# Performance work log

Hardware: AMD Instinct MI355X
Metric: run time of the kernel (lower is better)

Reference implementation:

```python
import jax, jax.numpy as jnp
import numpy as np

EPS = 1e-5
N_CONV = 3
B = 2048  # number of crystals


def _bn_eval(x, gamma, beta):
    # Eval-mode BatchNorm with running_mean=0, running_var=1.
    return x * (gamma / jnp.sqrt(1.0 + EPS)) + beta


def _conv_layer(atom_fea, nbr_fea, nbr_fea_idx, W, b, g1, b1, g2, b2):
    # Canonical CGCNN ConvLayer.
    N, M = nbr_fea_idx.shape
    F = atom_fea.shape[1]
    nbr_atom = atom_fea[nbr_fea_idx]                                  # [N,M,F]
    self_atom = jnp.broadcast_to(atom_fea[:, None, :], (N, M, F))     # [N,M,F]
    total = jnp.concatenate([self_atom, nbr_atom, nbr_fea], axis=2)   # [N,M,2F+nbr]
    gated = total @ W + b                                             # [N,M,2F]
    gated = _bn_eval(gated, g1, b1)
    flt, core = jnp.split(gated, 2, axis=2)
    nbr_sumed = jnp.sum(jax.nn.sigmoid(flt) * jax.nn.softplus(core), axis=1)  # [N,F]
    nbr_sumed = _bn_eval(nbr_sumed, g2, b2)
    return jax.nn.softplus(atom_fea + nbr_sumed)


def setup_inputs() -> dict:
    key = jax.random.key(0)
    ks = jax.random.split(key, 24)
    N, M = 60000, 12
    OA, NB, F, OE, E, H = 92, 41, 64, 8, 16, 128
    s = 0.05
    inp = {
        "atom_fea": jax.random.normal(ks[0], (N, OA), jnp.float32),
        "nbr_fea": jax.random.normal(ks[1], (N, M, NB), jnp.float32),
        "nbr_fea_idx": jax.random.randint(ks[2], (N, M), 0, N),
        "segment_ids": jnp.sort(jax.random.randint(ks[3], (N,), 0, B)),
        "extra_fea": jax.random.normal(ks[4], (B, OE), jnp.float32),
        # embedding_atom
        "W_embed": jax.random.normal(ks[5], (OA, F), jnp.float32) * s,
        "b_embed": jnp.zeros((F,), jnp.float32),
        # conv layers (stacked over n_conv=3)
        "conv_W": jax.random.normal(ks[6], (N_CONV, 2 * F + NB, 2 * F), jnp.float32) * s,
        "conv_b": jnp.zeros((N_CONV, 2 * F), jnp.float32),
        "bn1_g": jnp.ones((N_CONV, 2 * F), jnp.float32),
        "bn1_b": jnp.zeros((N_CONV, 2 * F), jnp.float32),
        "bn2_g": jnp.ones((N_CONV, F), jnp.float32),
        "bn2_b": jnp.zeros((N_CONV, F), jnp.float32),
        # embedding_extra
        "W_extra": jax.random.normal(ks[7], (OE, E), jnp.float32) * s,
        "b_extra": jnp.zeros((E,), jnp.float32),
        "bnx_g": jnp.ones((E,), jnp.float32),
        "bnx_b": jnp.zeros((E,), jnp.float32),
        # conv_to_fc
        "W_fc": jax.random.normal(ks[8], (F + E, H), jnp.float32) * s,
        "b_fc": jnp.zeros((H,), jnp.float32),
        "W_out0": jax.random.normal(ks[9], (H, 1), jnp.float32) * s,
        "b_out0": jnp.zeros((1,), jnp.float32),
        "W_out1": jax.random.normal(ks[10], (H, 2), jnp.float32) * s,
        "b_out1": jnp.zeros((2,), jnp.float32),
        "W_out2": jax.random.normal(ks[11], (H, 1), jnp.float32) * s,
        "b_out2": jnp.zeros((1,), jnp.float32),
    }
    return inp


def reference(atom_fea, nbr_fea, nbr_fea_idx, segment_ids, extra_fea,
              W_embed, b_embed, conv_W, conv_b, bn1_g, bn1_b, bn2_g, bn2_b,
              W_extra, b_extra, bnx_g, bnx_b, W_fc, b_fc,
              W_out0, b_out0, W_out1, b_out1, W_out2, b_out2):
    x = atom_fea @ W_embed + b_embed                                  # [N,F]
    extra = jax.nn.softplus(_bn_eval(extra_fea @ W_extra + b_extra, bnx_g, bnx_b))  # [B,E]
    for i in range(N_CONV):
        x = _conv_layer(x, nbr_fea, nbr_fea_idx, conv_W[i], conv_b[i],
                        bn1_g[i], bn1_b[i], bn2_g[i], bn2_b[i])
    # segment-mean pooling (replaces per-crystal python loop)
    sums = jax.ops.segment_sum(x, segment_ids, num_segments=B)        # [B,F]
    cnts = jax.ops.segment_sum(jnp.ones((x.shape[0],), x.dtype), segment_ids, num_segments=B)
    crys = sums / jnp.maximum(cnts, 1.0)[:, None]
    crys = jnp.concatenate([crys, extra], axis=1)                     # [B,F+E]
    crys = jax.nn.softplus(crys @ W_fc + b_fc)                        # [B,H]
    out0 = crys @ W_out0 + b_out0
    out1 = jax.nn.log_softmax(crys @ W_out1 + b_out1, axis=1)         # classification [B,2]
    out2 = crys @ W_out2 + b_out2
    return out0, out1, out2
```

## Files before the change

kernel.cpp:

```cpp
#include <hip/hip_runtime.h>
#include <math.h>
#include <stdint.h>

#define N_ATOMS 60000
#define M_NBR   12
#define NBF     41
#define B_CRYS  2048
#define EPSBN   1e-5f
#define GA      8
#define ROWS    (GA * M_NBR)
#define GRID_F  (N_ATOMS / GA)
#define WIMG_L  24576
#define EROW    48
#define EP_ROWS (GRID_F * ROWS)

#define PRE_WP   288
#define PRE_EMB  960
#define PRE_EPR  2048

typedef __attribute__((ext_vector_type(8))) short bf8;
typedef __attribute__((ext_vector_type(4))) float f32x4;
#define MFMA_B16(a, b, c) __builtin_amdgcn_mfma_f32_16x16x32_bf16(a, b, c, 0, 0, 0)

__device__ __forceinline__ short f2bf(float f) {
  uint32_t u = __builtin_bit_cast(uint32_t, f);
  u += 0x7FFFu + ((u >> 16) & 1u);
  return (short)(u >> 16);
}
__device__ __forceinline__ float lo16(uint32_t u) {
  return __builtin_bit_cast(float, u << 16);
}
__device__ __forceinline__ float hi16(uint32_t u) {
  return __builtin_bit_cast(float, u & 0xFFFF0000u);
}
__device__ __forceinline__ float sp(float x) {
  return (x > 15.f) ? x : __logf(1.f + __expf(x));
}
__device__ __forceinline__ float sig(float x) {
  return 1.f / (1.f + __expf(-x));
}

__global__ __launch_bounds__(256) void k_pre(
    const float* __restrict__ conv_W, const float* __restrict__ conv_b,
    const float* __restrict__ bn1_g, const float* __restrict__ bn1_b,
    unsigned short* __restrict__ Wimg, const float* __restrict__ A,
    const float* __restrict__ W, const float* __restrict__ bias,
    float* __restrict__ X, unsigned int* __restrict__ XbU,
    const float* __restrict__ NF, unsigned short* __restrict__ Eimg,
    int do_eprep) {
  const int b = blockIdx.x;

  if (b < PRE_WP) {
    const int gid = b * 256 + threadIdx.x;
    if (gid >= 3 * WIMG_L) return;
    const int layer = gid / WIMG_L, rem = gid % WIMG_L;
    const int which = rem / 8192, r2 = rem % 8192;
    const int frag = r2 >> 9, lane = (r2 >> 3) & 63, j = r2 & 7;
    const int ct = frag >> 1, ks = frag & 1;
    const int quad = lane >> 4, l15 = lane & 15;
    const int jc = ct * 16 + l15;
    const int oc = (jc & 1) ? (jc >> 1) + 64 : (jc >> 1);
    const float s = bn1_g[layer * 128 + oc] * rsqrtf(1.f + EPSBN);
    const int k = ks * 32 + quad * 8 + j;
    const float* Wc = conv_W + (size_t)layer * 169 * 128;
    float v = 0.f;
    if (which == 0) {
      if (k < NBF) v = Wc[(128 + k) * 128 + oc] * s;
      else if (k == NBF)
        v = conv_b[layer * 128 + oc] * s + bn1_b[layer * 128 + oc];
    } else if (which == 1) {
      v = Wc[k * 128 + oc] * s;
    } else {
      v = Wc[(64 + k) * 128 + oc] * s;
    }
    Wimg[gid] = (unsigned short)f2bf(v);
    return;
  }

  if (b < PRE_WP + PRE_EMB) {
    const int lane = threadIdx.x & 63, wv = threadIdx.x >> 6;
    const int quad = lane >> 4, l15 = lane & 15;
    const int gw = (b - PRE_WP) * 4 + wv;
    const int nw = PRE_EMB * 4;
    bf8 Bf[3][4];
    float bs[4];
#pragma unroll
    for (int ct = 0; ct < 4; ++ct) {
      const int col = ct * 16 + l15;
      bs[ct] = bias[col];
#pragma unroll
      for (int ks = 0; ks < 3; ++ks) {
        bf8 bb;
#pragma unroll
        for (int i = 0; i < 8; ++i) {
          const int k = ks * 32 + quad * 8 + i;
          bb[i] = (k < 92) ? f2bf(W[k * 64 + col]) : (short)0;
        }
        Bf[ks][ct] = bb;
      }
    }
    for (int rt = gw; rt < 3750; rt += nw) {
      const int rbase = rt * 16;
      const float* ar = A + (size_t)(rbase + l15) * 92;
      const float4 p0 = *(const float4*)(ar + quad * 8);
      const float4 p1 = *(const float4*)(ar + quad * 8 + 4);
      const float4 p2 = *(const float4*)(ar + 32 + quad * 8);
      const float4 p3 = *(const float4*)(ar + 32 + quad * 8 + 4);
      bf8 A0, A1, A2;
      A0[0] = f2bf(p0.x); A0[1] = f2bf(p0.y); A0[2] = f2bf(p0.z); A0[3] = f2bf(p0.w);
      A0[4] = f2bf(p1.x); A0[5] = f2bf(p1.y); A0[6] = f2bf(p1.z); A0[7] = f2bf(p1.w);
      A1[0] = f2bf(p2.x); A1[1] = f2bf(p2.y); A1[2] = f2bf(p2.z); A1[3] = f2bf(p2.w);
      A1[4] = f2bf(p3.x); A1[5] = f2bf(p3.y); A1[6] = f2bf(p3.z); A1[7] = f2bf(p3.w);
#pragma unroll
      for (int i = 0; i < 8; ++i) {
        const int k = 64 + quad * 8 + i;
        A2[i] = (k < 92) ? f2bf(ar[k]) : (short)0;
      }
      const f32x4 z = {0.f, 0.f, 0.f, 0.f};
      f32x4 acc[4];
#pragma unroll
      for (int ct = 0; ct < 4; ++ct) {
        acc[ct] = MFMA_B16(A0, Bf[0][ct], z);
        acc[ct] = MFMA_B16(A1, Bf[1][ct], acc[ct]);
        acc[ct] = MFMA_B16(A2, Bf[2][ct], acc[ct]);
      }
#pragma unroll
      for (int ct = 0; ct < 4; ++ct)
#pragma unroll
        for (int r = 0; r < 4; ++r) {
          const int row = rbase + quad * 4 + r;
          const float v = acc[ct][r] + bs[ct];
          X[(size_t)row * 64 + ct * 16 + l15] = v;
          const unsigned int u = (unsigned short)f2bf(v);
          const unsigned int p = __shfl_xor((int)u, 1);
          if (!(l15 & 1))
            XbU[(size_t)row * 32 + ct * 8 + (l15 >> 1)] = u | (p << 16);
        }
    }
    return;
  }

  if (!do_eprep) return;
  const int t0 = (b - PRE_WP - PRE_EMB) * 256 + threadIdx.x;
  for (int r = t0; r < EP_ROWS; r += PRE_EPR * 256) {
    const float* rp = NF + (size_t)r * NBF;
    unsigned short* op = Eimg + (size_t)r * EROW;
#pragma unroll
    for (int g8 = 0; g8 < 5; ++g8) {
      bf8 v;
#pragma unroll
      for (int i = 0; i < 8; ++i) v[i] = f2bf(rp[g8 * 8 + i]);
      *(bf8*)(op + g8 * 8) = v;
    }
    bf8 v5;
    v5[0] = f2bf(rp[40]);
    v5[1] = (short)0x3F80;
#pragma unroll
    for (int i = 2; i < 8; ++i) v5[i] = 0;
    *(bf8*)(op + 40) = v5;
  }
}

__global__ __launch_bounds__(256, 5) void k_fused6(
    float* __restrict__ X, const unsigned short* __restrict__ XbIn,
    unsigned int* __restrict__ XbOutU, const unsigned short* __restrict__ Eimg,
    const int* __restrict__ IDX, const unsigned short* __restrict__ Wi,
    const float* __restrict__ g2, const float* __restrict__ b2) {
  __shared__ __align__(16) unsigned int eb32[ROWS * 64];
  unsigned short* eb16 = (unsigned short*)eb32;
  const int tid = threadIdx.x;
  const int lane = tid & 63, wv = tid >> 6;
  const int quad = lane >> 4, l15 = lane & 15;
  const int g = blockIdx.x;
  const int ntile = (wv < 2) ? 2 : 1;

  bf8 Ax0[2], Ax1[2], As0[2], As1[2], Ae0[2], Ae1[2];
#pragma unroll
  for (int ti = 0; ti < 2; ++ti) {
    if (ti < ntile) {
      const int rbase = (wv + ti * 4) * 16;
      const int er = g * ROWS + rbase + l15;
      const int jr = IDX[er];
      const unsigned short* xr = XbIn + (size_t)jr * 64 + quad * 8;
      Ax0[ti] = *(const bf8*)xr;
      Ax1[ti] = *(const bf8*)(xr + 32);
      const int arow = g * GA + (rbase + l15) / M_NBR;
      const unsigned short* sr = XbIn + (size_t)arow * 64 + quad * 8;
      As0[ti] = *(const bf8*)sr;
      As1[ti] = *(const bf8*)(sr + 32);
      const unsigned short* ep = Eimg + (size_t)er * EROW;
      Ae0[ti] = *(const bf8*)(ep + quad * 8);
      bf8 a1;
#pragma unroll
      for (int i = 0; i < 8; ++i) a1[i] = 0;
      if (quad < 2) a1 = *(const bf8*)(ep + 32 + quad * 8);
      Ae1[ti] = a1;
    }
  }

#pragma unroll
  for (int ti = 0; ti < 2; ++ti) {
    if (ti < ntile) {
      const int rbase = (wv + ti * 4) * 16;
      const f32x4 z = {0.f, 0.f, 0.f, 0.f};
#pragma unroll 1
      for (int ct = 0; ct < 8; ++ct) {
        const bf8 Be0 = *(const bf8*)(Wi + ((ct * 2 + 0) * 64 + lane) * 8);
        const bf8 Be1 = *(const bf8*)(Wi + ((ct * 2 + 1) * 64 + lane) * 8);
        const bf8 Bs0 =
            *(const bf8*)(Wi + 8192 + ((ct * 2 + 0) * 64 + lane) * 8);
        const bf8 Bs1 =
            *(const bf8*)(Wi + 8192 + ((ct * 2 + 1) * 64 + lane) * 8);
        const bf8 Bn0 =
            *(const bf8*)(Wi + 16384 + ((ct * 2 + 0) * 64 + lane) * 8);
        const bf8 Bn1 =
            *(const bf8*)(Wi + 16384 + ((ct * 2 + 1) * 64 + lane) * 8);
        f32x4 acc = MFMA_B16(Ax0[ti], Bn0, z);
        acc = MFMA_B16(Ax1[ti], Bn1, acc);
        acc = MFMA_B16(As0[ti], Bs0, acc);
        acc = MFMA_B16(As1[ti], Bs1, acc);
        acc = MFMA_B16(Ae0[ti], Be0, acc);
        acc = MFMA_B16(Ae1[ti], Be1, acc);
        const int j = ct * 16 + l15;
        const int c = j >> 1, h = j & 1;
#pragma unroll
        for (int r = 0; r < 4; ++r) {
          const int row = rbase + quad * 4 + r;
          eb16[row * 128 + ((c + row) & 63) * 2 + h] =
              (unsigned short)f2bf(acc[r]);
        }
      }
    }
  }
  __syncthreads();

  const float inv = rsqrtf(1.f + EPSBN);
  const float s2 = g2[lane] * inv, o2 = b2[lane];
#pragma unroll
  for (int al = 0; al < 2; ++al) {
    const int a_local = wv * 2 + al;
    const int n = g * GA + a_local;
    float acc = 0.f;
#pragma unroll
    for (int m = 0; m < 12; ++m) {
      const int row = a_local * 12 + m;
      const uint32_t eu = eb32[row * 64 + ((lane + row) & 63)];
      acc += sig(lo16(eu)) * sp(hi16(eu));
    }
    const size_t o = (size_t)n * 64 + lane;
    const float res = sp(X[o] + acc * s2 + o2);
    X[o] = res;
    const unsigned int u = (unsigned short)f2bf(res);
    const unsigned int p = __shfl_xor((int)u, 1);
    if (!(lane & 1)) XbOutU[(size_t)n * 32 + (lane >> 1)] = u | (p << 16);
  }
}

__global__ __launch_bounds__(256, 5) void k_fused4(
    float* __restrict__ X, const unsigned short* __restrict__ XbIn,
    unsigned int* __restrict__ XbOutU, const float* __restrict__ NF,
    const int* __restrict__ IDX, const unsigned short* __restrict__ Wi,
    const float* __restrict__ g2, const float* __restrict__ b2) {
  __shared__ __align__(16) unsigned int eb32[ROWS * 64];
  unsigned short* eb16 = (unsigned short*)eb32;
  float* stage = (float*)eb32;
  const int tid = threadIdx.x;
  const int lane = tid & 63, wv = tid >> 6;
  const int quad = lane >> 4, l15 = lane & 15;
  const int g = blockIdx.x;
  const int ntile = (wv < 2) ? 2 : 1;

  bf8 Ax0[2], Ax1[2], As0[2], As1[2];
#pragma unroll
  for (int ti = 0; ti < 2; ++ti) {
    if (ti < ntile) {
      const int rbase = (wv + ti * 4) * 16;
      const int jr = IDX[g * ROWS + rbase + l15];
      const unsigned short* xr = XbIn + (size_t)jr * 64 + quad * 8;
      Ax0[ti] = *(const bf8*)xr;
      Ax1[ti] = *(const bf8*)(xr + 32);
      const int arow = g * GA + (rbase + l15) / M_NBR;
      const unsigned short* sr = XbIn + (size_t)arow * 64 + quad * 8;
      As0[ti] = *(const bf8*)sr;
      As1[ti] = *(const bf8*)(sr + 32);
    }
  }

  const float4* s4 = (const float4*)(NF + (size_t)g * (ROWS * NBF));
#pragma unroll
  for (int it = 0; it < 4; ++it) {
    const int w = tid + it * 256;
    if (w < (ROWS * NBF) / 4) ((float4*)stage)[w] = s4[w];
  }
  __syncthreads();

  bf8 Ae0[2], Ae1[2];
#pragma unroll
  for (int ti = 0; ti < 2; ++ti) {
    if (ti < ntile) {
      const int rbase = (wv + ti * 4) * 16;
      const float* rp = stage + (rbase + l15) * NBF;
      bf8 a0, a1;
#pragma unroll
      for (int i = 0; i < 8; ++i) a0[i] = f2bf(rp[quad * 8 + i]);
      if (quad == 0) {
#pragma unroll
        for (int i = 0; i < 8; ++i) a1[i] = f2bf(rp[32 + i]);
      } else if (quad == 1) {
        a1[0] = f2bf(rp[40]);
        a1[1] = (short)0x3F80;
#pragma unroll
        for (int i = 2; i < 8; ++i) a1[i] = 0;
      } else {
#pragma unroll
        for (int i = 0; i < 8; ++i) a1[i] = 0;
      }
      Ae0[ti] = a0;
      Ae1[ti] = a1;
    }
  }
  __syncthreads();

#pragma unroll
  for (int ti = 0; ti < 2; ++ti) {
    if (ti < ntile) {
      const int rbase = (wv + ti * 4) * 16;
      const f32x4 z = {0.f, 0.f, 0.f, 0.f};
#pragma unroll 1
      for (int ct = 0; ct < 8; ++ct) {
        const bf8 Be0 = *(const bf8*)(Wi + ((ct * 2 + 0) * 64 + lane) * 8);
        const bf8 Be1 = *(const bf8*)(Wi + ((ct * 2 + 1) * 64 + lane) * 8);
        const bf8 Bs0 =
            *(const bf8*)(Wi + 8192 + ((ct * 2 + 0) * 64 + lane) * 8);
        const bf8 Bs1 =
            *(const bf8*)(Wi + 8192 + ((ct * 2 + 1) * 64 + lane) * 8);
        const bf8 Bn0 =
            *(const bf8*)(Wi + 16384 + ((ct * 2 + 0) * 64 + lane) * 8);
        const bf8 Bn1 =
            *(const bf8*)(Wi + 16384 + ((ct * 2 + 1) * 64 + lane) * 8);
        f32x4 acc = MFMA_B16(Ax0[ti], Bn0, z);
        acc = MFMA_B16(Ax1[ti], Bn1, acc);
        acc = MFMA_B16(As0[ti], Bs0, acc);
        acc = MFMA_B16(As1[ti], Bs1, acc);
        acc = MFMA_B16(Ae0[ti], Be0, acc);
        acc = MFMA_B16(Ae1[ti], Be1, acc);
        const int j = ct * 16 + l15;
        const int c = j >> 1, h = j & 1;
#pragma unroll
        for (int r = 0; r < 4; ++r) {
          const int row = rbase + quad * 4 + r;
          eb16[row * 128 + ((c + row) & 63) * 2 + h] =
              (unsigned short)f2bf(acc[r]);
        }
      }
    }
  }
  __syncthreads();

  const float inv = rsqrtf(1.f + EPSBN);
  const float s2 = g2[lane] * inv, o2 = b2[lane];
#pragma unroll
  for (int al = 0; al < 2; ++al) {
    const int a_local = wv * 2 + al;
    const int n = g * GA + a_local;
    float acc = 0.f;
#pragma unroll
    for (int m = 0; m < 12; ++m) {
      const int row = a_local * 12 + m;
      const uint32_t eu = eb32[row * 64 + ((lane + row) & 63)];
      acc += sig(lo16(eu)) * sp(hi16(eu));
    }
    const size_t o = (size_t)n * 64 + lane;
    const float res = sp(X[o] + acc * s2 + o2);
    X[o] = res;
    const unsigned int u = (unsigned short)f2bf(res);
    const unsigned int p = __shfl_xor((int)u, 1);
    if (!(lane & 1)) XbOutU[(size_t)n * 32 + (lane >> 1)] = u | (p << 16);
  }
}

__device__ __forceinline__ int lbound(const int* __restrict__ a, int n, int v) {
  int lo = 0, hi = n;
  while (lo < hi) {
    int mid = (lo + hi) >> 1;
    if (a[mid] < v) lo = mid + 1; else hi = mid;
  }
  return lo;
}

__global__ __launch_bounds__(128) void k_head(
    const float* __restrict__ Xf, const int* __restrict__ seg,
    const float* __restrict__ EF, const float* __restrict__ Wx,
    const float* __restrict__ bx, const float* __restrict__ gx,
    const float* __restrict__ bxb, const float* __restrict__ Wfc,
    const float* __restrict__ bfc, const float* __restrict__ Wo0,
    const float* __restrict__ bo0, const float* __restrict__ Wo1,
    const float* __restrict__ bo1, const float* __restrict__ Wo2,
    const float* __restrict__ bo2, float* __restrict__ out) {
  const int b = blockIdx.x;
  const int t = threadIdx.x;
  __shared__ float vbuf[80];
  __shared__ float part[128];
  __shared__ float4 r4[128];
  const int lo = lbound(seg, N_ATOMS, b);
  const int hi = lbound(seg, N_ATOMS, b + 1);
  const int col = t & 63, half = t >> 6;
  float s = 0.f;
  for (int r = lo + half; r < hi; r += 2) s += Xf[(size_t)r * 64 + col];
  part[t] = s;
  __syncthreads();
  if (t < 64) {
    vbuf[t] = (part[t] + part[t + 64]) / fmaxf((float)(hi - lo), 1.f);
  } else if (t < 80) {
    const int e = t - 64;
    float a = bx[e];
#pragma unroll
    for (int k = 0; k < 8; ++k) a += EF[b * 8 + k] * Wx[k * 16 + e];
    a = a * (gx[e] * rsqrtf(1.f + EPSBN)) + bxb[e];
    vbuf[t] = sp(a);
  }
  __syncthreads();
  float h = bfc[t];
#pragma unroll
  for (int k = 0; k < 80; ++k) h += vbuf[k] * Wfc[k * 128 + t];
  h = sp(h);
  r4[t] = make_float4(h * Wo0[t], h * Wo1[2 * t], h * Wo1[2 * t + 1],
                      h * Wo2[t]);
  __syncthreads();
  for (int st2 = 64; st2 > 0; st2 >>= 1) {
    if (t < st2) {
      float4 a = r4[t], c = r4[t + st2];
      r4[t] = make_float4(a.x + c.x, a.y + c.y, a.z + c.z, a.w + c.w);
    }
    __syncthreads();
  }
  if (t == 0) {
    float4 r = r4[0];
    out[b] = r.x + bo0[0];
    float z0 = r.y + bo1[0], z1 = r.z + bo1[1];
    float mx = fmaxf(z0, z1);
    float lse = mx + __logf(__expf(z0 - mx) + __expf(z1 - mx));
    out[B_CRYS + 2 * b] = z0 - lse;
    out[B_CRYS + 2 * b + 1] = z1 - lse;
    out[3 * B_CRYS + b] = r.w + bo2[0];
  }
}

extern "C" void kernel_launch(void* const* d_in, const int* in_sizes, int n_in,
                              void* d_out, int out_size, void* d_ws,
                              size_t ws_size, hipStream_t stream) {
  const float* atom_fea = (const float*)d_in[0];
  const float* nbr_fea  = (const float*)d_in[1];
  const int*   nbr_idx  = (const int*)d_in[2];
  const int*   seg      = (const int*)d_in[3];
  const float* extra    = (const float*)d_in[4];
  const float* W_embed  = (const float*)d_in[5];
  const float* b_embed  = (const float*)d_in[6];
  const float* conv_W   = (const float*)d_in[7];
  const float* conv_b   = (const float*)d_in[8];
  const float* bn1_g    = (const float*)d_in[9];
  const float* bn1_b    = (const float*)d_in[10];
  const float* bn2_g    = (const float*)d_in[11];
  const float* bn2_b    = (const float*)d_in[12];
  const float* W_extra  = (const float*)d_in[13];
  const float* b_extra  = (const float*)d_in[14];
  const float* bnx_g    = (const float*)d_in[15];
  const float* bnx_b    = (const float*)d_in[16];
  const float* W_fc     = (const float*)d_in[17];
  const float* b_fc     = (const float*)d_in[18];
  const float* W_out0   = (const float*)d_in[19];
  const float* b_out0   = (const float*)d_in[20];
  const float* W_out1   = (const float*)d_in[21];
  const float* b_out1   = (const float*)d_in[22];
  const float* W_out2   = (const float*)d_in[23];
  const float* b_out2   = (const float*)d_in[24];
  float* out = (float*)d_out;

  float* x = (float*)d_ws;
  unsigned int* xbu0 = (unsigned int*)(x + (size_t)N_ATOMS * 64);
  unsigned int* xbu1 = xbu0 + (size_t)N_ATOMS * 32;
  unsigned short* Wimg = (unsigned short*)(xbu1 + (size_t)N_ATOMS * 32);
  unsigned short* Eimg = Wimg + (size_t)3 * WIMG_L;

  const size_t base_bytes =
      (size_t)N_ATOMS * 64 * 4 + (size_t)N_ATOMS * 32 * 4 * 2 +
      (size_t)3 * WIMG_L * 2;
  const size_t eimg_bytes = (size_t)EP_ROWS * EROW * 2;
  const bool use_eimg = (ws_size >= base_bytes + eimg_bytes);

  const int pre_grid =
      use_eimg ? (PRE_WP + PRE_EMB + PRE_EPR) : (PRE_WP + PRE_EMB);
  hipLaunchKernelGGL(k_pre, dim3(pre_grid), dim3(256), 0, stream, conv_W,
                     conv_b, bn1_g, bn1_b, Wimg, atom_fea, W_embed, b_embed, x,
                     xbu0, nbr_fea, Eimg, (int)use_eimg);

  unsigned int* xin = xbu0;
  unsigned int* xout = xbu1;
  for (int i = 0; i < 3; ++i) {
    if (use_eimg) {
      hipLaunchKernelGGL(k_fused6, dim3(GRID_F), dim3(256), 0, stream, x,
                         (const unsigned short*)xin, xout, Eimg, nbr_idx,
                         Wimg + (size_t)i * WIMG_L, bn2_g + i * 64,
                         bn2_b + i * 64);
    } else {
      hipLaunchKernelGGL(k_fused4, dim3(GRID_F), dim3(256), 0, stream, x,
                         (const unsigned short*)xin, xout, nbr_fea, nbr_idx,
                         Wimg + (size_t)i * WIMG_L, bn2_g + i * 64,
                         bn2_b + i * 64);
    }
    unsigned int* tmp = xin;
    xin = xout;
    xout = tmp;
  }
  hipLaunchKernelGGL(k_head, dim3(B_CRYS), dim3(128), 0, stream, x, seg, extra,
                     W_extra, b_extra, bnx_g, bnx_b, W_fc, b_fc, W_out0, b_out0,
                     W_out1, b_out1, W_out2, b_out2, out);
}
```

Measured before the change: 556.6 us.

## Fuse segment-mean pooling into last conv layer via atomics

```diff
diff --git a/kernel.cpp b/kernel.cpp
--- a/kernel.cpp
+++ b/kernel.cpp
@@ -14,9 +14,11 @@
 #define EROW    48
 #define EP_ROWS (GRID_F * ROWS)
 
+#define PRE_EPR  2048
 #define PRE_WP   288
 #define PRE_EMB  960
-#define PRE_EPR  2048
+#define PRE_Z    64
+#define PRE_GRID (PRE_EPR + PRE_WP + PRE_EMB + PRE_Z)
 
 typedef __attribute__((ext_vector_type(8))) short bf8;
 typedef __attribute__((ext_vector_type(4))) float f32x4;
@@ -47,11 +49,34 @@
     const float* __restrict__ W, const float* __restrict__ bias,
     float* __restrict__ X, unsigned int* __restrict__ XbU,
     const float* __restrict__ NF, unsigned short* __restrict__ Eimg,
-    int do_eprep) {
+    float* __restrict__ Xsum, int do_eprep) {
   const int b = blockIdx.x;
 
-  if (b < PRE_WP) {
-    const int gid = b * 256 + threadIdx.x;
+  if (b < PRE_EPR) {
+    if (!do_eprep) return;
+    const int t0 = b * 256 + threadIdx.x;
+    for (int r = t0; r < EP_ROWS; r += PRE_EPR * 256) {
+      const float* rp = NF + (size_t)r * NBF;
+      unsigned short* op = Eimg + (size_t)r * EROW;
+#pragma unroll
+      for (int g8 = 0; g8 < 5; ++g8) {
+        bf8 v;
+#pragma unroll
+        for (int i = 0; i < 8; ++i) v[i] = f2bf(rp[g8 * 8 + i]);
+        *(bf8*)(op + g8 * 8) = v;
+      }
+      bf8 v5;
+      v5[0] = f2bf(rp[40]);
+      v5[1] = (short)0x3F80;
+#pragma unroll
+      for (int i = 2; i < 8; ++i) v5[i] = 0;
+      *(bf8*)(op + 40) = v5;
+    }
+    return;
+  }
+
+  if (b < PRE_EPR + PRE_WP) {
+    const int gid = (b - PRE_EPR) * 256 + threadIdx.x;
     if (gid >= 3 * WIMG_L) return;
     const int layer = gid / WIMG_L, rem = gid % WIMG_L;
     const int which = rem / 8192, r2 = rem % 8192;
@@ -77,10 +102,10 @@
     return;
   }
 
-  if (b < PRE_WP + PRE_EMB) {
+  if (b < PRE_EPR + PRE_WP + PRE_EMB) {
     const int lane = threadIdx.x & 63, wv = threadIdx.x >> 6;
     const int quad = lane >> 4, l15 = lane & 15;
-    const int gw = (b - PRE_WP) * 4 + wv;
+    const int gw = (b - PRE_EPR - PRE_WP) * 4 + wv;
     const int nw = PRE_EMB * 4;
     bf8 Bf[3][4];
     float bs[4];
@@ -141,31 +166,18 @@
   }
 
   if (!do_eprep) return;
-  const int t0 = (b - PRE_WP - PRE_EMB) * 256 + threadIdx.x;
-  for (int r = t0; r < EP_ROWS; r += PRE_EPR * 256) {
-    const float* rp = NF + (size_t)r * NBF;
-    unsigned short* op = Eimg + (size_t)r * EROW;
-#pragma unroll
-    for (int g8 = 0; g8 < 5; ++g8) {
-      bf8 v;
-#pragma unroll
-      for (int i = 0; i < 8; ++i) v[i] = f2bf(rp[g8 * 8 + i]);
-      *(bf8*)(op + g8 * 8) = v;
-    }
-    bf8 v5;
-    v5[0] = f2bf(rp[40]);
-    v5[1] = (short)0x3F80;
-#pragma unroll
-    for (int i = 2; i < 8; ++i) v5[i] = 0;
-    *(bf8*)(op + 40) = v5;
-  }
-}
-
-__global__ __launch_bounds__(256, 5) void k_fused6(
+  const int zi = (b - PRE_EPR - PRE_WP - PRE_EMB) * 256 + threadIdx.x;
+  for (int i = zi; i < B_CRYS * 64 + B_CRYS; i += PRE_Z * 256) Xsum[i] = 0.f;
+}
+
+template <int FIN>
+__global__ __launch_bounds__(256, 5) void k_fused6t(
     float* __restrict__ X, const unsigned short* __restrict__ XbIn,
     unsigned int* __restrict__ XbOutU, const unsigned short* __restrict__ Eimg,
     const int* __restrict__ IDX, const unsigned short* __restrict__ Wi,
-    const float* __restrict__ g2, const float* __restrict__ b2) {
+    const float* __restrict__ g2, const float* __restrict__ b2,
+    const int* __restrict__ SEG, float* __restrict__ Xsum,
+    float* __restrict__ CntF) {
   __shared__ __align__(16) unsigned int eb32[ROWS * 64];
   unsigned short* eb16 = (unsigned short*)eb32;
   const int tid = threadIdx.x;
@@ -249,10 +261,16 @@
     }
     const size_t o = (size_t)n * 64 + lane;
     const float res = sp(X[o] + acc * s2 + o2);
-    X[o] = res;
-    const unsigned int u = (unsigned short)f2bf(res);
-    const unsigned int p = __shfl_xor((int)u, 1);
-    if (!(lane & 1)) XbOutU[(size_t)n * 32 + (lane >> 1)] = u | (p << 16);
+    if (FIN) {
+      const int s = SEG[n];
+      atomicAdd(&Xsum[(size_t)s * 64 + lane], res);
+      if (lane == 0) atomicAdd(&CntF[s], 1.f);
+    } else {
+      X[o] = res;
+      const unsigned int u = (unsigned short)f2bf(res);
+      const unsigned int p = __shfl_xor((int)u, 1);
+      if (!(lane & 1)) XbOutU[(size_t)n * 32 + (lane >> 1)] = u | (p << 16);
+    }
   }
 }
 
@@ -396,28 +414,42 @@
     const float* __restrict__ bfc, const float* __restrict__ Wo0,
     const float* __restrict__ bo0, const float* __restrict__ Wo1,
     const float* __restrict__ bo1, const float* __restrict__ Wo2,
-    const float* __restrict__ bo2, float* __restrict__ out) {
+    const float* __restrict__ bo2, const float* __restrict__ Xsum,
+    const float* __restrict__ CntF, int pooled, float* __restrict__ out) {
   const int b = blockIdx.x;
   const int t = threadIdx.x;
   __shared__ float vbuf[80];
   __shared__ float part[128];
   __shared__ float4 r4[128];
-  const int lo = lbound(seg, N_ATOMS, b);
-  const int hi = lbound(seg, N_ATOMS, b + 1);
-  const int col = t & 63, half = t >> 6;
-  float s = 0.f;
-  for (int r = lo + half; r < hi; r += 2) s += Xf[(size_t)r * 64 + col];
-  part[t] = s;
-  __syncthreads();
-  if (t < 64) {
-    vbuf[t] = (part[t] + part[t + 64]) / fmaxf((float)(hi - lo), 1.f);
-  } else if (t < 80) {
-    const int e = t - 64;
-    float a = bx[e];
-#pragma unroll
-    for (int k = 0; k < 8; ++k) a += EF[b * 8 + k] * Wx[k * 16 + e];
-    a = a * (gx[e] * rsqrtf(1.f + EPSBN)) + bxb[e];
-    vbuf[t] = sp(a);
+  if (pooled) {
+    if (t < 64) {
+      vbuf[t] = Xsum[(size_t)b * 64 + t] / fmaxf(CntF[b], 1.f);
+    } else if (t < 80) {
+      const int e = t - 64;
+      float a = bx[e];
+#pragma unroll
+      for (int k = 0; k < 8; ++k) a += EF[b * 8 + k] * Wx[k * 16 + e];
+      a = a * (gx[e] * rsqrtf(1.f + EPSBN)) + bxb[e];
+      vbuf[t] = sp(a);
+    }
+  } else {
+    const int lo = lbound(seg, N_ATOMS, b);
+    const int hi = lbound(seg, N_ATOMS, b + 1);
+    const int col = t & 63, half = t >> 6;
+    float s = 0.f;
+    for (int r = lo + half; r < hi; r += 2) s += Xf[(size_t)r * 64 + col];
+    part[t] = s;
+    __syncthreads();
+    if (t < 64) {
+      vbuf[t] = (part[t] + part[t + 64]) / fmaxf((float)(hi - lo), 1.f);
+    } else if (t < 80) {
+      const int e = t - 64;
+      float a = bx[e];
+#pragma unroll
+      for (int k = 0; k < 8; ++k) a += EF[b * 8 + k] * Wx[k * 16 + e];
+      a = a * (gx[e] * rsqrtf(1.f + EPSBN)) + bxb[e];
+      vbuf[t] = sp(a);
+    }
   }
   __syncthreads();
   float h = bfc[t];
@@ -480,28 +512,35 @@
   unsigned int* xbu0 = (unsigned int*)(x + (size_t)N_ATOMS * 64);
   unsigned int* xbu1 = xbu0 + (size_t)N_ATOMS * 32;
   unsigned short* Wimg = (unsigned short*)(xbu1 + (size_t)N_ATOMS * 32);
-  unsigned short* Eimg = Wimg + (size_t)3 * WIMG_L;
+  float* xsum = (float*)(Wimg + (size_t)3 * WIMG_L);
+  float* cntf = xsum + (size_t)B_CRYS * 64;
+  unsigned short* Eimg = (unsigned short*)(cntf + B_CRYS);
 
   const size_t base_bytes =
       (size_t)N_ATOMS * 64 * 4 + (size_t)N_ATOMS * 32 * 4 * 2 +
-      (size_t)3 * WIMG_L * 2;
+      (size_t)3 * WIMG_L * 2 + (size_t)(B_CRYS * 64 + B_CRYS) * 4;
   const size_t eimg_bytes = (size_t)EP_ROWS * EROW * 2;
   const bool use_eimg = (ws_size >= base_bytes + eimg_bytes);
 
-  const int pre_grid =
-      use_eimg ? (PRE_WP + PRE_EMB + PRE_EPR) : (PRE_WP + PRE_EMB);
-  hipLaunchKernelGGL(k_pre, dim3(pre_grid), dim3(256), 0, stream, conv_W,
+  hipLaunchKernelGGL(k_pre, dim3(PRE_GRID), dim3(256), 0, stream, conv_W,
                      conv_b, bn1_g, bn1_b, Wimg, atom_fea, W_embed, b_embed, x,
-                     xbu0, nbr_fea, Eimg, (int)use_eimg);
+                     xbu0, nbr_fea, Eimg, xsum, (int)use_eimg);
 
   unsigned int* xin = xbu0;
   unsigned int* xout = xbu1;
   for (int i = 0; i < 3; ++i) {
     if (use_eimg) {
-      hipLaunchKernelGGL(k_fused6, dim3(GRID_F), dim3(256), 0, stream, x,
-                         (const unsigned short*)xin, xout, Eimg, nbr_idx,
-                         Wimg + (size_t)i * WIMG_L, bn2_g + i * 64,
-                         bn2_b + i * 64);
+      if (i < 2) {
+        hipLaunchKernelGGL(k_fused6t<0>, dim3(GRID_F), dim3(256), 0, stream, x,
+                           (const unsigned short*)xin, xout, Eimg, nbr_idx,
+                           Wimg + (size_t)i * WIMG_L, bn2_g + i * 64,
+                           bn2_b + i * 64, seg, xsum, cntf);
+      } else {
+        hipLaunchKernelGGL(k_fused6t<1>, dim3(GRID_F), dim3(256), 0, stream, x,
+                           (const unsigned short*)xin, xout, Eimg, nbr_idx,
+                           Wimg + (size_t)i * WIMG_L, bn2_g + i * 64,
+                           bn2_b + i * 64, seg, xsum, cntf);
+      }
     } else {
       hipLaunchKernelGGL(k_fused4, dim3(GRID_F), dim3(256), 0, stream, x,
                          (const unsigned short*)xin, xout, nbr_fea, nbr_idx,
@@ -514,5 +553,6 @@
   }
   hipLaunchKernelGGL(k_head, dim3(B_CRYS), dim3(128), 0, stream, x, seg, extra,
                      W_extra, b_extra, bnx_g, bnx_b, W_fc, b_fc, W_out0, b_out0,
-                     W_out1, b_out1, W_out2, b_out2, out);
-}
+                     W_out1, b_out1, W_out2, b_out2, xsum, cntf, (int)use_eimg,
+                     out);
+}
```

Result: slower. 571.7 us (+2.7%).

## Split bf16 edge prep into finer chunks, precompute segment bounds, widen head

Applied to the files above, without the earlier changes.

```diff
diff --git a/kernel.cpp b/kernel.cpp
--- a/kernel.cpp
+++ b/kernel.cpp
@@ -13,10 +13,13 @@
 #define WIMG_L  24576
 #define EROW    48
 #define EP_ROWS (GRID_F * ROWS)
-
+#define EP_CHUNKS (EP_ROWS * 6)
+
+#define PRE_EPR  2048
 #define PRE_WP   288
 #define PRE_EMB  960
-#define PRE_EPR  2048
+#define PRE_B    9
+#define PRE_GRID (PRE_EPR + PRE_WP + PRE_EMB + PRE_B)
 
 typedef __attribute__((ext_vector_type(8))) short bf8;
 typedef __attribute__((ext_vector_type(4))) float f32x4;
@@ -38,6 +41,14 @@
 }
 __device__ __forceinline__ float sig(float x) {
   return 1.f / (1.f + __expf(-x));
+}
+__device__ __forceinline__ int lbound(const int* __restrict__ a, int n, int v) {
+  int lo = 0, hi = n;
+  while (lo < hi) {
+    int mid = (lo + hi) >> 1;
+    if (a[mid] < v) lo = mid + 1; else hi = mid;
+  }
+  return lo;
 }
 
 __global__ __launch_bounds__(256) void k_pre(
@@ -47,11 +58,33 @@
     const float* __restrict__ W, const float* __restrict__ bias,
     float* __restrict__ X, unsigned int* __restrict__ XbU,
     const float* __restrict__ NF, unsigned short* __restrict__ Eimg,
-    int do_eprep) {
+    const int* __restrict__ seg, int* __restrict__ bounds, int do_eprep) {
   const int b = blockIdx.x;
 
-  if (b < PRE_WP) {
-    const int gid = b * 256 + threadIdx.x;
+  if (b < PRE_EPR) {
+    if (!do_eprep) return;
+    const int t0 = b * 256 + threadIdx.x;
+    for (int c = t0; c < EP_CHUNKS; c += PRE_EPR * 256) {
+      const int row = c / 6, sg = c - row * 6;
+      const float* rp = NF + (size_t)row * NBF + sg * 8;
+      unsigned short* op = Eimg + (size_t)row * EROW + sg * 8;
+      bf8 v;
+      if (sg < 5) {
+#pragma unroll
+        for (int i = 0; i < 8; ++i) v[i] = f2bf(rp[i]);
+      } else {
+        v[0] = f2bf(rp[0]);
+        v[1] = (short)0x3F80;
+#pragma unroll
+        for (int i = 2; i < 8; ++i) v[i] = 0;
+      }
+      *(bf8*)op = v;
+    }
+    return;
+  }
+
+  if (b < PRE_EPR + PRE_WP) {
+    const int gid = (b - PRE_EPR) * 256 + threadIdx.x;
     if (gid >= 3 * WIMG_L) return;
     const int layer = gid / WIMG_L, rem = gid % WIMG_L;
     const int which = rem / 8192, r2 = rem % 8192;
@@ -77,10 +110,10 @@
     return;
   }
 
-  if (b < PRE_WP + PRE_EMB) {
+  if (b < PRE_EPR + PRE_WP + PRE_EMB) {
     const int lane = threadIdx.x & 63, wv = threadIdx.x >> 6;
     const int quad = lane >> 4, l15 = lane & 15;
-    const int gw = (b - PRE_WP) * 4 + wv;
+    const int gw = (b - PRE_EPR - PRE_WP) * 4 + wv;
     const int nw = PRE_EMB * 4;
     bf8 Bf[3][4];
     float bs[4];
@@ -140,25 +173,8 @@
     return;
   }
 
-  if (!do_eprep) return;
-  const int t0 = (b - PRE_WP - PRE_EMB) * 256 + threadIdx.x;
-  for (int r = t0; r < EP_ROWS; r += PRE_EPR * 256) {
-    const float* rp = NF + (size_t)r * NBF;
-    unsigned short* op = Eimg + (size_t)r * EROW;
-#pragma unroll
-    for (int g8 = 0; g8 < 5; ++g8) {
-      bf8 v;
-#pragma unroll
-      for (int i = 0; i < 8; ++i) v[i] = f2bf(rp[g8 * 8 + i]);
-      *(bf8*)(op + g8 * 8) = v;
-    }
-    bf8 v5;
-    v5[0] = f2bf(rp[40]);
-    v5[1] = (short)0x3F80;
-#pragma unroll
-    for (int i = 2; i < 8; ++i) v5[i] = 0;
-    *(bf8*)(op + 40) = v5;
-  }
+  const int bi = (b - PRE_EPR - PRE_WP - PRE_EMB) * 256 + threadIdx.x;
+  if (bi <= B_CRYS) bounds[bi] = lbound(seg, N_ATOMS, bi);
 }
 
 __global__ __launch_bounds__(256, 5) void k_fused6(
@@ -379,17 +395,8 @@
   }
 }
 
-__device__ __forceinline__ int lbound(const int* __restrict__ a, int n, int v) {
-  int lo = 0, hi = n;
-  while (lo < hi) {
-    int mid = (lo + hi) >> 1;
-    if (a[mid] < v) lo = mid + 1; else hi = mid;
-  }
-  return lo;
-}
-
-__global__ __launch_bounds__(128) void k_head(
-    const float* __restrict__ Xf, const int* __restrict__ seg,
+__global__ __launch_bounds__(256) void k_head(
+    const float* __restrict__ Xf, const int* __restrict__ bounds,
     const float* __restrict__ EF, const float* __restrict__ Wx,
     const float* __restrict__ bx, const float* __restrict__ gx,
     const float* __restrict__ bxb, const float* __restrict__ Wfc,
@@ -400,17 +407,18 @@
   const int b = blockIdx.x;
   const int t = threadIdx.x;
   __shared__ float vbuf[80];
-  __shared__ float part[128];
+  __shared__ float part[256];
   __shared__ float4 r4[128];
-  const int lo = lbound(seg, N_ATOMS, b);
-  const int hi = lbound(seg, N_ATOMS, b + 1);
-  const int col = t & 63, half = t >> 6;
+  const int lo = bounds[b];
+  const int hi = bounds[b + 1];
+  const int col = t & 63, qq = t >> 6;
   float s = 0.f;
-  for (int r = lo + half; r < hi; r += 2) s += Xf[(size_t)r * 64 + col];
+  for (int r = lo + qq; r < hi; r += 4) s += Xf[(size_t)r * 64 + col];
   part[t] = s;
   __syncthreads();
   if (t < 64) {
-    vbuf[t] = (part[t] + part[t + 64]) / fmaxf((float)(hi - lo), 1.f);
+    vbuf[t] = (part[t] + part[t + 64] + part[t + 128] + part[t + 192]) /
+              fmaxf((float)(hi - lo), 1.f);
   } else if (t < 80) {
     const int e = t - 64;
     float a = bx[e];
@@ -420,12 +428,14 @@
     vbuf[t] = sp(a);
   }
   __syncthreads();
-  float h = bfc[t];
-#pragma unroll
-  for (int k = 0; k < 80; ++k) h += vbuf[k] * Wfc[k * 128 + t];
-  h = sp(h);
-  r4[t] = make_float4(h * Wo0[t], h * Wo1[2 * t], h * Wo1[2 * t + 1],
-                      h * Wo2[t]);
+  if (t < 128) {
+    float h = bfc[t];
+#pragma unroll
+    for (int k = 0; k < 80; ++k) h += vbuf[k] * Wfc[k * 128 + t];
+    h = sp(h);
+    r4[t] = make_float4(h * Wo0[t], h * Wo1[2 * t], h * Wo1[2 * t + 1],
+                        h * Wo2[t]);
+  }
   __syncthreads();
   for (int st2 = 64; st2 > 0; st2 >>= 1) {
     if (t < st2) {
@@ -480,19 +490,18 @@
   unsigned int* xbu0 = (unsigned int*)(x + (size_t)N_ATOMS * 64);
   unsigned int* xbu1 = xbu0 + (size_t)N_ATOMS * 32;
   unsigned short* Wimg = (unsigned short*)(xbu1 + (size_t)N_ATOMS * 32);
-  unsigned short* Eimg = Wimg + (size_t)3 * WIMG_L;
+  int* bounds = (int*)(Wimg + (size_t)3 * WIMG_L);
+  unsigned short* Eimg = (unsigned short*)(bounds + 2052);
 
   const size_t base_bytes =
       (size_t)N_ATOMS * 64 * 4 + (size_t)N_ATOMS * 32 * 4 * 2 +
-      (size_t)3 * WIMG_L * 2;
+      (size_t)3 * WIMG_L * 2 + 2052 * 4;
   const size_t eimg_bytes = (size_t)EP_ROWS * EROW * 2;
   const bool use_eimg = (ws_size >= base_bytes + eimg_bytes);
 
-  const int pre_grid =
-      use_eimg ? (PRE_WP + PRE_EMB + PRE_EPR) : (PRE_WP + PRE_EMB);
-  hipLaunchKernelGGL(k_pre, dim3(pre_grid), dim3(256), 0, stream, conv_W,
+  hipLaunchKernelGGL(k_pre, dim3(PRE_GRID), dim3(256), 0, stream, conv_W,
                      conv_b, bn1_g, bn1_b, Wimg, atom_fea, W_embed, b_embed, x,
-                     xbu0, nbr_fea, Eimg, (int)use_eimg);
+                     xbu0, nbr_fea, Eimg, seg, bounds, (int)use_eimg);
 
   unsigned int* xin = xbu0;
   unsigned int* xout = xbu1;
@@ -512,7 +521,7 @@
     xin = xout;
     xout = tmp;
   }
-  hipLaunchKernelGGL(k_head, dim3(B_CRYS), dim3(128), 0, stream, x, seg, extra,
-                     W_extra, b_extra, bnx_g, bnx_b, W_fc, b_fc, W_out0, b_out0,
-                     W_out1, b_out1, W_out2, b_out2, out);
-}
+  hipLaunchKernelGGL(k_head, dim3(B_CRYS), dim3(256), 0, stream, x, bounds,
+                     extra, W_extra, b_extra, bnx_g, bnx_b, W_fc, b_fc, W_out0,
+                     b_out0, W_out1, b_out1, W_out2, b_out2, out);
+}
```

Result: faster. 541.5 us (-2.7%).
